# Performance work log

Measured on AMD Instinct MI355X. Metric: run time of the kernel, lower is better.

## Reference

```python
import jax, jax.numpy as jnp
import numpy as np

B, S, D, H = 2, 2048, 1024, 16
DH = D // H
SCALE = 1.0 / float(np.sqrt(DH))


def setup_inputs() -> dict:
    key = jax.random.key(0)
    ks = jax.random.split(key, 9)
    std = 1.0 / float(np.sqrt(D))
    x = jax.random.normal(ks[0], (B, S, D), dtype=jnp.float32)
    # causal mask: True = masked (future positions)
    mask = jnp.triu(jnp.ones((S, S), dtype=bool), k=1)
    Wq = jax.random.normal(ks[1], (D, D), dtype=jnp.float32) * std
    Wk = jax.random.normal(ks[2], (D, D), dtype=jnp.float32) * std
    Wv = jax.random.normal(ks[3], (D, D), dtype=jnp.float32) * std
    Wo = jax.random.normal(ks[4], (D, D), dtype=jnp.float32) * std
    bq = jax.random.normal(ks[5], (D,), dtype=jnp.float32) * 0.01
    bk = jax.random.normal(ks[6], (D,), dtype=jnp.float32) * 0.01
    bv = jax.random.normal(ks[7], (D,), dtype=jnp.float32) * 0.01
    bo = jax.random.normal(ks[8], (D,), dtype=jnp.float32) * 0.01
    return {"x": x, "mask": mask, "Wq": Wq, "bq": bq, "Wk": Wk, "bk": bk,
            "Wv": Wv, "bv": bv, "Wo": Wo, "bo": bo}


def _split_heads(t):
    # (B, S, D) -> (B, H, S, DH)
    return t.reshape(B, S, H, DH).transpose(0, 2, 1, 3)


def reference(x, mask, Wq, bq, Wk, bk, Wv, bv, Wo, bo):
    # torch nn.Linear: y = x @ W.T + b
    q = _split_heads(x @ Wq.T + bq)
    k = _split_heads(x @ Wk.T + bk)
    v = _split_heads(x @ Wv.T + bv)
    # scores: (B, H, S, S)
    scores = jnp.einsum('bhsd,bhtd->bhst', q, k) * SCALE
    scores = jnp.where(mask[None, None, :, :], jnp.float32(-1e9), scores)
    attn = jax.nn.softmax(scores, axis=-1)
    attn = jnp.nan_to_num(attn, nan=0.0)
    out = jnp.einsum('bhst,bhtd->bhsd', attn, v)
    out = out.transpose(0, 2, 1, 3).reshape(B, S, D)
    return out @ Wo.T + bo
```

## Files before the change

kernel.cpp:

```cpp
#include <hip/hip_runtime.h>

#define S_LEN  2048
#define DMODEL 1024
#define NHEAD  16
#define DHEAD  64
#define SCALE_F 0.125f
#define SL2E_F 0.180336880f

typedef unsigned short ushort_t;
typedef __attribute__((ext_vector_type(8))) short bf16x8;
typedef __attribute__((ext_vector_type(4))) float f32x4;

typedef __attribute__((address_space(1))) void gv_t;
typedef __attribute__((address_space(3))) void lv_t;

__device__ __forceinline__ ushort_t f2bf(float f) {
    unsigned u = __builtin_bit_cast(unsigned, f);
    unsigned r = (u + 0x7FFFu + ((u >> 16) & 1u)) >> 16;
    return (ushort_t)r;
}

__device__ __forceinline__ unsigned cvtpk_bf16(float a, float b) {
    unsigned r;
    asm("v_cvt_pk_bf16_f32 %0, %1, %2" : "=v"(r) : "v"(a), "v"(b));
    return r;
}

__device__ __forceinline__ void gload16(const ushort_t* g, ushort_t* l) {
    __builtin_amdgcn_global_load_lds((gv_t*)g, (lv_t*)l, 16, 0, 0);
}

__global__ void cast_all(const float* __restrict__ x,
                         const float* __restrict__ Wq, const float* __restrict__ Wk,
                         const float* __restrict__ Wv, const float* __restrict__ Wo,
                         ushort_t* __restrict__ dst, int n4) {
    int i = blockIdx.x * blockDim.x + threadIdx.x;
    int stride = gridDim.x * blockDim.x;
    for (int idx = i; idx < n4; idx += stride) {
        const float* src; int off;
        if (idx < 1048576)      { src = x;  off = idx; }
        else if (idx < 1310720) { src = Wq; off = idx - 1048576; }
        else if (idx < 1572864) { src = Wk; off = idx - 1310720; }
        else if (idx < 1835008) { src = Wv; off = idx - 1572864; }
        else                    { src = Wo; off = idx - 1835008; }
        float4 f = ((const float4*)src)[off];
        ushort4 o;
        o.x = f2bf(f.x); o.y = f2bf(f.y); o.z = f2bf(f.z); o.w = f2bf(f.w);
        ((ushort4*)dst)[idx] = o;
    }
}

template<int MODE, int BM>
__launch_bounds__(256)
__global__ void gemm_bt(const ushort_t* __restrict__ A, const ushort_t* __restrict__ Bw,
                        const float* __restrict__ b0, const float* __restrict__ b1,
                        const float* __restrict__ b2,
                        void* __restrict__ out0, void* __restrict__ out1, void* __restrict__ out2,
                        int M, int N, int K) {
    constexpr int MF = BM / 32;
    __shared__ ushort_t As[2][BM][32];
    __shared__ ushort_t Bs[2][128][32];
    const int tid  = threadIdx.x;
    const int lane = tid & 63;
    const int w    = tid >> 6;
    const int wr   = w >> 1, wc = w & 1;
    const int m0   = blockIdx.x * BM;
    const int n0   = blockIdx.y * 128;
    const int l15  = lane & 15;
    const int lg   = lane >> 4;
    const int srow = lane >> 2;
    const int scol = (lane & 3) * 8;

    f32x4 acc[MF][4] = {};

    auto stage = [&](int buf, int k0) {
#pragma unroll
        for (int j = 0; j < BM / 64; j++) {
            const int rbase = w * (BM / 4) + j * 16;
            gload16(A + (size_t)(m0 + rbase + srow) * K + k0 + scol, &As[buf][rbase][0]);
        }
#pragma unroll
        for (int j = 0; j < 2; j++) {
            const int rbase = w * 32 + j * 16;
            gload16(Bw + (size_t)(n0 + rbase + srow) * K + k0 + scol, &Bs[buf][rbase][0]);
        }
    };

    stage(0, 0);
    __syncthreads();
    int buf = 0;

    for (int k0 = 0; k0 < K; k0 += 32) {
        if (k0 + 32 < K) stage(buf ^ 1, k0 + 32);
        bf16x8 af[MF], bfr[4];
#pragma unroll
        for (int i = 0; i < MF; i++) af[i]  = *(const bf16x8*)&As[buf][wr*(BM/2) + i*16 + l15][lg*8];
#pragma unroll
        for (int i = 0; i < 4;  i++) bfr[i] = *(const bf16x8*)&Bs[buf][wc*64 + i*16 + l15][lg*8];
#pragma unroll
        for (int mf = 0; mf < MF; mf++)
#pragma unroll
            for (int nf = 0; nf < 4; nf++)
                acc[mf][nf] = __builtin_amdgcn_mfma_f32_16x16x32_bf16(af[mf], bfr[nf], acc[mf][nf], 0, 0, 0);
        __syncthreads();
        buf ^= 1;
    }

#pragma unroll
    for (int mf = 0; mf < MF; mf++) {
#pragma unroll
        for (int nf = 0; nf < 4; nf++) {
            const int col = n0 + wc*64 + nf*16 + l15;
            if constexpr (MODE == 2) {
                const float bv = b0[col];
#pragma unroll
                for (int r = 0; r < 4; r++) {
                    const int row = m0 + wr*(BM/2) + mf*16 + lg*4 + r;
                    ((float*)out0)[(size_t)row * N + col] = acc[mf][nf][r] + bv;
                }
            } else {
                const int mat = col >> 10;
                const int c   = col & 1023;
                const int h   = c >> 6, dh = c & 63;
                const float* bp = (mat == 0) ? b0 : ((mat == 1) ? b1 : b2);
                const float bv = bp[c];
#pragma unroll
                for (int r = 0; r < 4; r++) {
                    const int row = m0 + wr*(BM/2) + mf*16 + lg*4 + r;
                    const int b = row >> 11, s = row & 2047;
                    float v = acc[mf][nf][r] + bv;
                    if (mat == 0) {
                        v *= SL2E_F;
                        ((ushort_t*)out0)[((size_t)(b*NHEAD + h) * S_LEN + s) * DHEAD + dh] = f2bf(v);
                    } else if (mat == 1)
                        ((ushort_t*)out1)[((size_t)(b*NHEAD + h) * S_LEN + s) * DHEAD + dh] = f2bf(v);
                    else
                        ((ushort_t*)out2)[((size_t)(b*NHEAD + h) * DHEAD + dh) * S_LEN + s] = f2bf(v);
                }
            }
        }
    }
}

__launch_bounds__(256, 4)
__global__ void attn_fwd(const ushort_t* __restrict__ Q, const ushort_t* __restrict__ Kh,
                         const ushort_t* __restrict__ Vt, ushort_t* __restrict__ Aout) {
    __shared__ ushort_t Ks[2][64][64];
    __shared__ ushort_t Vs[2][64][64];
    __shared__ ushort_t Ps[4][16][64];
    const int tid  = threadIdx.x;
    const int lane = tid & 63;
    const int w    = tid >> 6;
    const int l15  = lane & 15, lg = lane >> 4;
    const int bh   = blockIdx.x;
    const int y    = blockIdx.y;
    const int kq   = y >> 3, g0 = y & 7;
    const int qt   = (kq == 0) ? 2*g0 : (kq == 1) ? (31 - 2*g0)
                   : (kq == 2) ? (2*g0 + 1) : (30 - 2*g0);

    const size_t qkbase = (size_t)bh * S_LEN * DHEAD;
    const size_t vtbase = (size_t)bh * DHEAD * S_LEN;

    const int rsub  = lane >> 3;
    const int csw   = ((lane & 7) ^ rsub) * 8;
    const int swz   = (l15 & 7) * 8;
    const int psxor = (l15 & 7) << 4;

    const int qw = qt * 64 + w * 16;

    bf16x8 aq[2];
#pragma unroll
    for (int kc = 0; kc < 2; kc++)
        aq[kc] = *(const bf16x8*)(Q + qkbase + (size_t)(qw + l15) * DHEAD + kc*32 + lg*8);

    float m = -3.0e38f, l = 0.0f;
    f32x4 o[4] = {};

    auto stage = [&](int buf, int t) {
        const int kv0 = t * 64;
        const ushort_t* kp = Kh + qkbase + (size_t)kv0 * DHEAD;
        const ushort_t* vp = Vt + vtbase + kv0;
#pragma unroll
        for (int j2 = 0; j2 < 2; j2++) {
            const int j  = w * 2 + j2;
            const int rg = j * 8 + rsub;
            gload16(kp + (size_t)rg * DHEAD + csw, &Ks[buf][j*8][0]);
            gload16(vp + (size_t)rg * S_LEN + csw, &Vs[buf][j*8][0]);
        }
    };

    ushort_t* psw = &Ps[w][0][0];
    char* psrow = (char*)(psw + l15 * 64);

    stage(0, 0);
    __syncthreads();
    int buf = 0;

    for (int t = 0; t <= qt; t++) {
        if (t < qt) stage(buf ^ 1, t + 1);

        f32x4 sacc[4] = {};
        __builtin_amdgcn_s_setprio(1);
#pragma unroll
        for (int kc = 0; kc < 2; kc++)
#pragma unroll
            for (int nf = 0; nf < 4; nf++) {
                bf16x8 bk = *(const bf16x8*)&Ks[buf][nf*16 + l15][(kc*32 + lg*8) ^ swz];
                sacc[nf] = __builtin_amdgcn_mfma_f32_16x16x32_bf16(bk, aq[kc], sacc[nf], 0, 0, 0);
            }
        __builtin_amdgcn_s_setprio(0);

        if (t == qt) {
            const int rowq = qw + l15;
            const int kv0  = t * 64;
#pragma unroll
            for (int nf = 0; nf < 4; nf++)
#pragma unroll
                for (int r = 0; r < 4; r++) {
                    const int colk = kv0 + nf*16 + lg*4 + r;
                    if (colk > rowq) sacc[nf][r] = -3.0e38f;
                }
        }

        float mnf[4];
#pragma unroll
        for (int nf = 0; nf < 4; nf++)
            mnf[nf] = fmaxf(fmaxf(sacc[nf][0], sacc[nf][1]), fmaxf(sacc[nf][2], sacc[nf][3]));
        float mx = fmaxf(fmaxf(mnf[0], mnf[1]), fmaxf(mnf[2], mnf[3]));
        mx = fmaxf(mx, __shfl_xor(mx, 16));
        mx = fmaxf(mx, __shfl_xor(mx, 32));

        const bool skip = __all(mx <= m + 8.0f);
        const float mn = skip ? m : fmaxf(m, mx);

        float snf[4];
#pragma unroll
        for (int nf = 0; nf < 4; nf++) {
            const float p0 = exp2f(sacc[nf][0] - mn);
            const float p1 = exp2f(sacc[nf][1] - mn);
            const float p2 = exp2f(sacc[nf][2] - mn);
            const float p3 = exp2f(sacc[nf][3] - mn);
            uint2 pk;
            pk.x = cvtpk_bf16(p0, p1);
            pk.y = cvtpk_bf16(p2, p3);
            *(uint2*)(psrow + (((nf*16 + lg*4) * 2) ^ psxor)) = pk;
            snf[nf] = (p0 + p1) + (p2 + p3);
        }
        float s = (snf[0] + snf[1]) + (snf[2] + snf[3]);
        s += __shfl_xor(s, 16);
        s += __shfl_xor(s, 32);

        if (skip) {
            l += s;
        } else {
            const float corr = exp2f(m - mn);
            m = mn;
            l = l * corr + s;
            float cf[4];
#pragma unroll
            for (int r = 0; r < 4; r++) cf[r] = __shfl(corr, lg*4 + r);
#pragma unroll
            for (int nf = 0; nf < 4; nf++)
#pragma unroll
                for (int r = 0; r < 4; r++) o[nf][r] *= cf[r];
        }

        __builtin_amdgcn_s_setprio(1);
#pragma unroll
        for (int kc = 0; kc < 2; kc++) {
            bf16x8 pa = *(const bf16x8*)(psrow + (((kc*32 + lg*8) * 2) ^ psxor));
#pragma unroll
            for (int nf = 0; nf < 4; nf++) {
                bf16x8 bv = *(const bf16x8*)&Vs[buf][nf*16 + l15][(kc*32 + lg*8) ^ swz];
                o[nf] = __builtin_amdgcn_mfma_f32_16x16x32_bf16(pa, bv, o[nf], 0, 0, 0);
            }
        }
        __builtin_amdgcn_s_setprio(0);

        __syncthreads();
        buf ^= 1;
    }

    const int b = bh >> 4, h = bh & 15;
    const float inv = 1.0f / l;
#pragma unroll
    for (int r = 0; r < 4; r++) {
        const float ia = __shfl(inv, lg*4 + r);
        const int rowq = qw + lg*4 + r;
#pragma unroll
        for (int nf = 0; nf < 4; nf++)
            Aout[((size_t)(b * S_LEN) + rowq) * DMODEL + h*DHEAD + nf*16 + l15] = f2bf(o[nf][r] * ia);
    }
}

extern "C" void kernel_launch(void* const* d_in, const int* in_sizes, int n_in,
                              void* d_out, int out_size, void* d_ws, size_t ws_size,
                              hipStream_t stream) {
    (void)in_sizes; (void)n_in; (void)out_size; (void)ws_size;
    const float* x  = (const float*)d_in[0];
    const float* Wq = (const float*)d_in[2];
    const float* bq = (const float*)d_in[3];
    const float* Wk = (const float*)d_in[4];
    const float* bk = (const float*)d_in[5];
    const float* Wv = (const float*)d_in[6];
    const float* bv = (const float*)d_in[7];
    const float* Wo = (const float*)d_in[8];
    const float* bo = (const float*)d_in[9];

    char* ws = (char*)d_ws;
    ushort_t* xb    = (ushort_t*)(ws);
    ushort_t* Wqkvb = (ushort_t*)(ws + (8u  << 20));
    ushort_t* Wob   = (ushort_t*)(ws + (14u << 20));
    ushort_t* Qh    = (ushort_t*)(ws + (16u << 20));
    ushort_t* Kh    = (ushort_t*)(ws + (24u << 20));
    ushort_t* Vth   = (ushort_t*)(ws + (32u << 20));
    ushort_t* Ao    = (ushort_t*)(ws + (40u << 20));

    cast_all<<<2048, 256, 0, stream>>>(x, Wq, Wk, Wv, Wo, xb, 2097152);

    gemm_bt<0, 128><<<dim3(32, 24), 256, 0, stream>>>(xb, Wqkvb, bq, bk, bv,
                                                      Qh, Kh, Vth, 2*S_LEN, 3*DMODEL, DMODEL);

    attn_fwd<<<dim3(2*NHEAD, 32), 256, 0, stream>>>(Qh, Kh, Vth, Ao);

    gemm_bt<2, 64><<<dim3(64, 8), 256, 0, stream>>>(Ao, Wob, bo, nullptr, nullptr,
                                                    d_out, nullptr, nullptr, 2*S_LEN, DMODEL, DMODEL);
}
```

Before: 115.2 us.

## Deepen GEMM K-tile with swizzled LDS and fine-grained vmcnt waits for overlap

```diff
diff --git a/kernel.cpp b/kernel.cpp
--- a/kernel.cpp
+++ b/kernel.cpp
@@ -28,6 +28,13 @@
 
 __device__ __forceinline__ void gload16(const ushort_t* g, ushort_t* l) {
     __builtin_amdgcn_global_load_lds((gv_t*)g, (lv_t*)l, 16, 0, 0);
+}
+
+template<int N> __device__ __forceinline__ void wait_vmcnt() {
+    if constexpr (N == 8)      asm volatile("s_waitcnt vmcnt(8)" ::: "memory");
+    else if constexpr (N == 6) asm volatile("s_waitcnt vmcnt(6)" ::: "memory");
+    else if constexpr (N == 4) asm volatile("s_waitcnt vmcnt(4)" ::: "memory");
+    else                       asm volatile("s_waitcnt vmcnt(0)" ::: "memory");
 }
 
 __global__ void cast_all(const float* __restrict__ x,
@@ -58,8 +65,9 @@
                         void* __restrict__ out0, void* __restrict__ out1, void* __restrict__ out2,
                         int M, int N, int K) {
     constexpr int MF = BM / 32;
-    __shared__ ushort_t As[2][BM][32];
-    __shared__ ushort_t Bs[2][128][32];
+    constexpr int NLOADS = BM / 32 + 4;
+    __shared__ ushort_t As[2][BM][64];
+    __shared__ ushort_t Bs[2][128][64];
     const int tid  = threadIdx.x;
     const int lane = tid & 63;
     const int w    = tid >> 6;
@@ -68,41 +76,65 @@
     const int n0   = blockIdx.y * 128;
     const int l15  = lane & 15;
     const int lg   = lane >> 4;
-    const int srow = lane >> 2;
-    const int scol = (lane & 3) * 8;
+    const int srow8 = lane >> 3;
+    const int scol8 = ((lane & 7) ^ srow8) * 8;
 
     f32x4 acc[MF][4] = {};
 
     auto stage = [&](int buf, int k0) {
 #pragma unroll
-        for (int j = 0; j < BM / 64; j++) {
-            const int rbase = w * (BM / 4) + j * 16;
-            gload16(A + (size_t)(m0 + rbase + srow) * K + k0 + scol, &As[buf][rbase][0]);
-        }
-#pragma unroll
-        for (int j = 0; j < 2; j++) {
-            const int rbase = w * 32 + j * 16;
-            gload16(Bw + (size_t)(n0 + rbase + srow) * K + k0 + scol, &Bs[buf][rbase][0]);
+        for (int j = 0; j < BM / 32; j++) {
+            const int rg = (w * (BM / 32) + j) * 8;
+            gload16(A + (size_t)(m0 + rg + srow8) * K + k0 + scol8, &As[buf][rg][0]);
+        }
+#pragma unroll
+        for (int j = 0; j < 4; j++) {
+            const int rg = (w * 4 + j) * 8;
+            gload16(Bw + (size_t)(n0 + rg + srow8) * K + k0 + scol8, &Bs[buf][rg][0]);
         }
     };
 
     stage(0, 0);
-    __syncthreads();
     int buf = 0;
 
-    for (int k0 = 0; k0 < K; k0 += 32) {
-        if (k0 + 32 < K) stage(buf ^ 1, k0 + 32);
-        bf16x8 af[MF], bfr[4];
-#pragma unroll
-        for (int i = 0; i < MF; i++) af[i]  = *(const bf16x8*)&As[buf][wr*(BM/2) + i*16 + l15][lg*8];
-#pragma unroll
-        for (int i = 0; i < 4;  i++) bfr[i] = *(const bf16x8*)&Bs[buf][wc*64 + i*16 + l15][lg*8];
-#pragma unroll
-        for (int mf = 0; mf < MF; mf++)
-#pragma unroll
-            for (int nf = 0; nf < 4; nf++)
-                acc[mf][nf] = __builtin_amdgcn_mfma_f32_16x16x32_bf16(af[mf], bfr[nf], acc[mf][nf], 0, 0, 0);
-        __syncthreads();
+    for (int k0 = 0; k0 < K; k0 += 64) {
+        if (k0 + 64 < K) {
+            stage(buf ^ 1, k0 + 64);
+            wait_vmcnt<NLOADS>();
+        } else {
+            wait_vmcnt<0>();
+        }
+        __builtin_amdgcn_s_barrier();
+        __builtin_amdgcn_sched_barrier(0);
+
+        bf16x8 af[MF][2], bfr[4][2];
+#pragma unroll
+        for (int i = 0; i < MF; i++) {
+            const int row = wr * (BM / 2) + i * 16 + l15;
+#pragma unroll
+            for (int kk = 0; kk < 2; kk++)
+                af[i][kk] = *(const bf16x8*)&As[buf][row][((kk*4 + lg) ^ (l15 & 7)) * 8];
+        }
+#pragma unroll
+        for (int i = 0; i < 4; i++) {
+            const int row = wc * 64 + i * 16 + l15;
+#pragma unroll
+            for (int kk = 0; kk < 2; kk++)
+                bfr[i][kk] = *(const bf16x8*)&Bs[buf][row][((kk*4 + lg) ^ (l15 & 7)) * 8];
+        }
+        __builtin_amdgcn_s_setprio(1);
+#pragma unroll
+        for (int kk = 0; kk < 2; kk++)
+#pragma unroll
+            for (int mf = 0; mf < MF; mf++)
+#pragma unroll
+                for (int nf = 0; nf < 4; nf++)
+                    acc[mf][nf] = __builtin_amdgcn_mfma_f32_16x16x32_bf16(af[mf][kk], bfr[nf][kk], acc[mf][nf], 0, 0, 0);
+        __builtin_amdgcn_s_setprio(0);
+
+        asm volatile("s_waitcnt lgkmcnt(0)" ::: "memory");
+        __builtin_amdgcn_sched_barrier(0);
+        __builtin_amdgcn_s_barrier();
         buf ^= 1;
     }
 
@@ -193,11 +225,17 @@
     char* psrow = (char*)(psw + l15 * 64);
 
     stage(0, 0);
-    __syncthreads();
     int buf = 0;
 
     for (int t = 0; t <= qt; t++) {
-        if (t < qt) stage(buf ^ 1, t + 1);
+        if (t < qt) {
+            stage(buf ^ 1, t + 1);
+            wait_vmcnt<4>();
+        } else {
+            wait_vmcnt<0>();
+        }
+        __builtin_amdgcn_s_barrier();
+        __builtin_amdgcn_sched_barrier(0);
 
         f32x4 sacc[4] = {};
         __builtin_amdgcn_s_setprio(1);
@@ -277,7 +315,9 @@
         }
         __builtin_amdgcn_s_setprio(0);
 
-        __syncthreads();
+        asm volatile("s_waitcnt lgkmcnt(0)" ::: "memory");
+        __builtin_amdgcn_sched_barrier(0);
+        __builtin_amdgcn_s_barrier();
         buf ^= 1;
     }
 
```

New measurement: 120.9 us. 1.05x slower.
